# Kernel tuning notes

Hardware: AMD Instinct MI355X
Metric: run time of the kernel (lower is better)

Reference implementation:

```python
import jax, jax.numpy as jnp
import numpy as np

N = 131072   # active input voxels (stride=1 -> same output voxels)
K = 27       # 3x3x3 kernel offsets
P = 32768    # padded kernel-map pairs per offset
CIN = 64
COUT = 64


def setup_inputs() -> dict:
    key = jax.random.key(0)
    kf, kw, kb, ki, ko, km = jax.random.split(key, 6)
    features = jax.random.normal(kf, (N, CIN), jnp.float32)
    weight = jax.random.normal(kw, (K, CIN, COUT), jnp.float32) * 0.05
    bias = jax.random.normal(kb, (COUT,), jnp.float32)
    # kernel map: per-offset (input_row, output_row) pairs, -1 = padding
    in_map = jax.random.randint(ki, (K, P), 0, N, dtype=jnp.int32)
    out_map = jax.random.randint(ko, (K, P), 0, N, dtype=jnp.int32)
    valid = jax.random.uniform(km, (K, P)) < 0.8
    in_map = jnp.where(valid, in_map, -1)
    out_map = jnp.where(valid, out_map, -1)
    return {"features": features, "weight": weight, "bias": bias,
            "in_map": in_map, "out_map": out_map}


def reference(features, weight, bias, in_map, out_map):
    # Sparse conv = per-offset gather -> GEMM -> scatter-add, plus bias.
    valid = in_map >= 0                                   # [K, P]
    safe_in = jnp.where(valid, in_map, 0)
    gathered = features[safe_in] * valid[:, :, None].astype(features.dtype)  # [K,P,Cin]
    y = jnp.einsum('kpi,kio->kpo', gathered, weight)      # [K,P,Cout]
    safe_out = jnp.where(valid, out_map, 0).reshape(-1)   # invalid rows carry zeros
    out = jnp.zeros((features.shape[0], weight.shape[-1]), features.dtype)
    out = out.at[safe_out].add(y.reshape(-1, weight.shape[-1]))
    return out + bias[None, :]
```

## Files before the change

kernel.cpp:

```cpp
#include <hip/hip_runtime.h>
#include <hip/hip_bf16.h>

#define NVOX 131072
#define KOFF 27
#define PPAIR 32768
#define CIN 64
#define COUT 64
#define PPB 128
#define FS 72
#define TOTP (KOFF * PPAIR)
#define CAP 12
#define OVF_MAX 32768

typedef __attribute__((ext_vector_type(8))) short bf16x8;
typedef __attribute__((ext_vector_type(4))) float f32x4;
typedef __attribute__((ext_vector_type(4))) unsigned int u32x4;
typedef __attribute__((ext_vector_type(2))) unsigned int u32x2;

static constexpr size_t WIMG_BYTES = (size_t)KOFF * COUT * FS * 2;
static constexpr size_t FB_BYTES   = ((size_t)NVOX + 1) * CIN * 2;

static constexpr size_t YC_OFF    = 0;
static constexpr size_t YC_BYTES  = (size_t)NVOX * CAP * COUT * 2;
static constexpr size_t CUR2_OFF  = YC_OFF + YC_BYTES;
static constexpr size_t OVFC_OFF  = CUR2_OFF + (size_t)NVOX * 4;
static constexpr size_t OVF_OFF   = OVFC_OFF + 256;
static constexpr size_t WIMG2_OFF = OVF_OFF + (size_t)OVF_MAX * 4;
static constexpr size_t FB2_OFF   = (WIMG2_OFF + WIMG_BYTES + 255) & ~(size_t)255;
static constexpr size_t WS_CAP    = FB2_OFF + FB_BYTES;

static constexpr size_t Y_OFF     = 0;
static constexpr size_t Y_BYTES   = (size_t)TOTP * COUT * 2;
static constexpr size_t RANK_OFF  = Y_OFF + Y_BYTES;
static constexpr size_t CNT_OFF   = RANK_OFF + (size_t)TOTP * 4;
static constexpr size_t START_OFF = CNT_OFF + (size_t)NVOX * 4;
static constexpr size_t BSUM_OFF  = START_OFF + ((size_t)NVOX + 64) * 4;
static constexpr size_t BOFF_OFF  = BSUM_OFF + 512 * 4;
static constexpr size_t WIMG_OFF  = BOFF_OFF + 520 * 4;
static constexpr size_t FB_OFF    = (WIMG_OFF + WIMG_BYTES + 255) & ~(size_t)255;
static constexpr size_t WS_FULL   = FB_OFF + FB_BYTES;

__device__ __forceinline__ unsigned short f2bf(float f) {
    union { __hip_bfloat16 h; unsigned short u; } v;
    v.h = __float2bfloat16(f);
    return v.u;
}
__device__ __forceinline__ float bfbits2f(unsigned int u) {
    union { unsigned int i; float f; } v; v.i = u << 16; return v.f;
}
__device__ __forceinline__ float dot8(u32x4 a, u32x4 b) {
    float s = 0.f;
    s += bfbits2f(a.x & 0xffffu) * bfbits2f(b.x & 0xffffu);
    s += bfbits2f(a.x >> 16)     * bfbits2f(b.x >> 16);
    s += bfbits2f(a.y & 0xffffu) * bfbits2f(b.y & 0xffffu);
    s += bfbits2f(a.y >> 16)     * bfbits2f(b.y >> 16);
    s += bfbits2f(a.z & 0xffffu) * bfbits2f(b.z & 0xffffu);
    s += bfbits2f(a.z >> 16)     * bfbits2f(b.z >> 16);
    s += bfbits2f(a.w & 0xffffu) * bfbits2f(b.w & 0xffffu);
    s += bfbits2f(a.w >> 16)     * bfbits2f(b.w >> 16);
    return s;
}

#define NB_F2B 4096
#define NB_WP  KOFF
#define NB_RNK (TOTP / 256)

__global__ __launch_bounds__(256) void prep2_kernel(
    const float* __restrict__ f, unsigned short* __restrict__ fb,
    const float* __restrict__ w, unsigned short* __restrict__ wimg)
{
    const int bid = blockIdx.x;
    const int tid = threadIdx.x;
    if (bid < NB_F2B) {
        int i = bid * 256 + tid;
        float4 a = ((const float4*)f)[i * 2];
        float4 b = ((const float4*)f)[i * 2 + 1];
        union { u32x4 u; unsigned short s[8]; } pk;
        pk.s[0]=f2bf(a.x); pk.s[1]=f2bf(a.y); pk.s[2]=f2bf(a.z); pk.s[3]=f2bf(a.w);
        pk.s[4]=f2bf(b.x); pk.s[5]=f2bf(b.y); pk.s[6]=f2bf(b.z); pk.s[7]=f2bf(b.w);
        ((u32x4*)fb)[i] = pk.u;
    } else {
        const int k    = bid - NB_F2B;
        const int cout = tid & 63;
        const int ci0  = (tid >> 6) * 16;
        const float* wk = w + (size_t)k * CIN * COUT;
        union { u32x4 u[2]; unsigned short s[16]; } pk;
#pragma unroll
        for (int i = 0; i < 16; ++i)
            pk.s[i] = f2bf(wk[(ci0 + i) * COUT + cout]);
        unsigned short* dst = wimg + (size_t)k * COUT * FS + cout * FS + ci0;
        *(u32x4*)dst       = pk.u[0];
        *(u32x4*)(dst + 8) = pk.u[1];
        if (k == 0 && tid < CIN) fb[(size_t)NVOX * CIN + tid] = 0;
    }
}

__global__ __launch_bounds__(256) void conv5_kernel(
    const unsigned short* __restrict__ featbf,
    const unsigned short* __restrict__ wimg,
    const int* __restrict__ in_map,
    const int* __restrict__ out_map,
    int* __restrict__ cursor,
    int* __restrict__ ovf_cnt,
    int* __restrict__ ovf,
    unsigned short* __restrict__ Ybf)
{
    __shared__ unsigned short Fl[PPB * FS];
    __shared__ unsigned short Wt[COUT * FS];

    const int tid  = threadIdx.x;
    const int wave = tid >> 6;
    const int lane = tid & 63;
    const int k    = blockIdx.x >> 8;
    const int pb   = blockIdx.x & 255;
    const int base = k * PPAIR + pb * PPB;

    const int p = tid >> 1;
    const int h = tid & 1;
    int slot = -1;
    {
        int o = out_map[base + p];
        if (h == 0 && o >= 0) {
            int r0 = atomicAdd(&cursor[o], 1);
            if (r0 < CAP) {
                slot = o * CAP + r0;
            } else {
                int idx = atomicAdd(ovf_cnt, 1);
                if (idx < OVF_MAX) ovf[idx] = base + p;
            }
        }
    }

    {
        const unsigned short* wsrc = wimg + (size_t)k * COUT * FS;
        for (int c = wave; c < 9; c += 4)
            __builtin_amdgcn_global_load_lds(
                (const __attribute__((address_space(1))) void*)(wsrc + c * 512 + lane * 8),
                (__attribute__((address_space(3))) void*)(&Wt[c * 512 + lane * 8]),
                16, 0, 0);
    }

    {
        int im = in_map[base + p];
        const u32x4* src = (const u32x4*)(featbf + (size_t)(im >= 0 ? im : NVOX) * CIN + h * 32);
        u32x4 v0 = src[0], v1 = src[1], v2 = src[2], v3 = src[3];
        u32x4* dst = (u32x4*)&Fl[p * FS + h * 32];
        dst[0] = v0; dst[1] = v1; dst[2] = v2; dst[3] = v3;
    }

    slot = __shfl(slot, lane & 62);

    __syncthreads();

    const int r = lane & 15;
    const int g = lane >> 4;

    bf16x8 af[2][2];
    bf16x8 bfr[4][2];
#pragma unroll
    for (int m = 0; m < 2; ++m)
#pragma unroll
        for (int s = 0; s < 2; ++s)
            af[m][s] = *(const bf16x8*)&Fl[(wave * 32 + m * 16 + r) * FS + s * 32 + g * 8];
#pragma unroll
    for (int n = 0; n < 4; ++n)
#pragma unroll
        for (int s = 0; s < 2; ++s)
            bfr[n][s] = *(const bf16x8*)&Wt[(n * 16 + r) * FS + s * 32 + g * 8];

    f32x4 acc[2][4];
#pragma unroll
    for (int m = 0; m < 2; ++m)
#pragma unroll
        for (int n = 0; n < 4; ++n)
            acc[m][n] = (f32x4){0.f, 0.f, 0.f, 0.f};

#pragma unroll
    for (int s = 0; s < 2; ++s)
#pragma unroll
        for (int m = 0; m < 2; ++m)
#pragma unroll
            for (int n = 0; n < 4; ++n)
                acc[m][n] = __builtin_amdgcn_mfma_f32_16x16x32_bf16(
                    af[m][s], bfr[n][s], acc[m][n], 0, 0, 0);

#pragma unroll
    for (int m = 0; m < 2; ++m)
#pragma unroll
        for (int n = 0; n < 4; ++n)
#pragma unroll
            for (int j = 0; j < 4; ++j)
                Fl[(wave * 32 + m * 16 + g * 4 + j) * FS + n * 16 + r] = f2bf(acc[m][n][j]);

    if (slot >= 0) {
        const unsigned short* src = &Fl[p * FS + h * 32];
        u32x4* dst = (u32x4*)(Ybf + (size_t)slot * COUT + h * 32);
        u32x4 v0 = *(const u32x4*)(src + 0);
        u32x4 v1 = *(const u32x4*)(src + 8);
        u32x4 v2 = *(const u32x4*)(src + 16);
        u32x4 v3 = *(const u32x4*)(src + 24);
        dst[0] = v0; dst[1] = v1; dst[2] = v2; dst[3] = v3;
    }
}

__global__ __launch_bounds__(256) void gather_cap_kernel(
    const unsigned short* __restrict__ Y,
    const int* __restrict__ cursor,
    const float* __restrict__ bias,
    float* __restrict__ out)
{
    const int row  = blockIdx.x * 4 + (threadIdx.x >> 6);
    const int lane = threadIdx.x & 63;
    const int c4   = (lane & 15) * 4;
    const int grp  = lane >> 4;

    int cnt = cursor[row];
    if (cnt > CAP) cnt = CAP;
    const unsigned short* yb = Y + (size_t)row * CAP * COUT;

    float4 acc = {0.f, 0.f, 0.f, 0.f};
    for (int j = grp; j < cnt; j += 4) {
        u32x2 v = *(const u32x2*)&yb[j * COUT + c4];
        acc.x += bfbits2f(v.x & 0xffffu);
        acc.y += bfbits2f(v.x >> 16);
        acc.z += bfbits2f(v.y & 0xffffu);
        acc.w += bfbits2f(v.y >> 16);
    }
    acc.x += __shfl_xor(acc.x, 16); acc.y += __shfl_xor(acc.y, 16);
    acc.z += __shfl_xor(acc.z, 16); acc.w += __shfl_xor(acc.w, 16);
    acc.x += __shfl_xor(acc.x, 32); acc.y += __shfl_xor(acc.y, 32);
    acc.z += __shfl_xor(acc.z, 32); acc.w += __shfl_xor(acc.w, 32);

    if (grp == 0) {
        float4 b = *(const float4*)&bias[c4];
        float4 rv = {acc.x + b.x, acc.y + b.y, acc.z + b.z, acc.w + b.w};
        *(float4*)&out[(size_t)row * COUT + c4] = rv;
    }
}

__global__ __launch_bounds__(256) void fixup_kernel(
    const unsigned short* __restrict__ fb,
    const unsigned short* __restrict__ wimg,
    const int* __restrict__ in_map,
    const int* __restrict__ out_map,
    const int* __restrict__ ovf_cnt,
    const int* __restrict__ ovf,
    float* __restrict__ out)
{
    int n = ovf_cnt[0];
    if (n > OVF_MAX) n = OVF_MAX;
    const int lane = threadIdx.x & 63;
    const int wid  = (blockIdx.x * 256 + threadIdx.x) >> 6;
    const int nw   = (gridDim.x * 256) >> 6;
    for (int e = wid; e < n; e += nw) {
        int t  = ovf[e];
        int k  = t >> 15;
        int in = in_map[t];
        int o  = out_map[t];
        const u32x4* fr = (const u32x4*)(fb + (size_t)in * CIN);
        const unsigned short* wr = wimg + (size_t)k * COUT * FS + lane * FS;
        float acc = 0.f;
#pragma unroll
        for (int c8 = 0; c8 < 8; ++c8)
            acc += dot8(fr[c8], *(const u32x4*)(wr + c8 * 8));
        unsafeAtomicAdd(out + (size_t)o * COUT + lane, acc);
    }
}

__global__ __launch_bounds__(256) void prep_kernel(
    const float* __restrict__ f, unsigned short* __restrict__ fb,
    const float* __restrict__ w, unsigned short* __restrict__ wimg,
    const int* __restrict__ out_map, int* __restrict__ counts,
    int* __restrict__ rank)
{
    const int bid = blockIdx.x;
    const int tid = threadIdx.x;
    if (bid < NB_F2B) {
        int i = bid * 256 + tid;
        float4 a = ((const float4*)f)[i * 2];
        float4 b = ((const float4*)f)[i * 2 + 1];
        union { u32x4 u; unsigned short s[8]; } pk;
        pk.s[0]=f2bf(a.x); pk.s[1]=f2bf(a.y); pk.s[2]=f2bf(a.z); pk.s[3]=f2bf(a.w);
        pk.s[4]=f2bf(b.x); pk.s[5]=f2bf(b.y); pk.s[6]=f2bf(b.z); pk.s[7]=f2bf(b.w);
        ((u32x4*)fb)[i] = pk.u;
    } else if (bid < NB_F2B + NB_WP) {
        const int k    = bid - NB_F2B;
        const int cout = tid & 63;
        const int ci0  = (tid >> 6) * 16;
        const float* wk = w + (size_t)k * CIN * COUT;
        union { u32x4 u[2]; unsigned short s[16]; } pk;
#pragma unroll
        for (int i = 0; i < 16; ++i)
            pk.s[i] = f2bf(wk[(ci0 + i) * COUT + cout]);
        unsigned short* dst = wimg + (size_t)k * COUT * FS + cout * FS + ci0;
        *(u32x4*)dst       = pk.u[0];
        *(u32x4*)(dst + 8) = pk.u[1];
        if (k == 0 && tid < CIN) fb[(size_t)NVOX * CIN + tid] = 0;
    } else {
        int t = (bid - NB_F2B - NB_WP) * 256 + tid;
        int o = out_map[t];
        rank[t] = (o >= 0) ? atomicAdd(&counts[o], 1) : -1;
    }
}

__global__ void scan1_kernel(const int* __restrict__ counts, int* __restrict__ startv,
                             int* __restrict__ bsum) {
    __shared__ int sm[256];
    int gid = blockIdx.x * 256 + threadIdx.x;
    int v = counts[gid];
    sm[threadIdx.x] = v;
    __syncthreads();
    for (int off = 1; off < 256; off <<= 1) {
        int t = (threadIdx.x >= off) ? sm[threadIdx.x - off] : 0;
        __syncthreads();
        sm[threadIdx.x] += t;
        __syncthreads();
    }
    int incl = sm[threadIdx.x];
    startv[gid] = incl - v;
    if (threadIdx.x == 255) bsum[blockIdx.x] = incl;
}

__global__ void scan2_kernel(const int* __restrict__ bsum, int* __restrict__ boff) {
    __shared__ int sm[512];
    int v = bsum[threadIdx.x];
    sm[threadIdx.x] = v;
    __syncthreads();
    for (int off = 1; off < 512; off <<= 1) {
        int t = (threadIdx.x >= off) ? sm[threadIdx.x - off] : 0;
        __syncthreads();
        sm[threadIdx.x] += t;
        __syncthreads();
    }
    boff[threadIdx.x] = sm[threadIdx.x] - v;
    if (threadIdx.x == 511) boff[512] = sm[511];
}

__global__ __launch_bounds__(256) void conv4_kernel(
    const unsigned short* __restrict__ featbf,
    const unsigned short* __restrict__ wimg,
    const int* __restrict__ in_map,
    const int* __restrict__ out_map,
    const int* __restrict__ startv,
    const int* __restrict__ boff,
    const int* __restrict__ rank,
    unsigned short* __restrict__ Ybf)
{
    __shared__ unsigned short Fl[PPB * FS];
    __shared__ unsigned short Wt[COUT * FS];

    const int tid  = threadIdx.x;
    const int wave = tid >> 6;
    const int lane = tid & 63;
    const int k    = blockIdx.x >> 8;
    const int pb   = blockIdx.x & 255;
    const int base = k * PPAIR + pb * PPB;

    {
        const unsigned short* wsrc = wimg + (size_t)k * COUT * FS;
        for (int c = wave; c < 9; c += 4)
            __builtin_amdgcn_global_load_lds(
                (const __attribute__((address_space(1))) void*)(wsrc + c * 512 + lane * 8),
                (__attribute__((address_space(3))) void*)(&Wt[c * 512 + lane * 8]),
                16, 0, 0);
    }
    {
        const int row = tid >> 1;
        const int h   = tid & 1;
        int im = in_map[base + row];
        const u32x4* src = (const u32x4*)(featbf + (size_t)(im >= 0 ? im : NVOX) * CIN + h * 32);
        u32x4 v0 = src[0], v1 = src[1], v2 = src[2], v3 = src[3];
        u32x4* dst = (u32x4*)&Fl[row * FS + h * 32];
        dst[0] = v0; dst[1] = v1; dst[2] = v2; dst[3] = v3;
    }
    __syncthreads();

    const int r = lane & 15;
    const int g = lane >> 4;

    bf16x8 af[2][2];
    bf16x8 bfr[4][2];
#pragma unroll
    for (int m = 0; m < 2; ++m)
#pragma unroll
        for (int s = 0; s < 2; ++s)
            af[m][s] = *(const bf16x8*)&Fl[(wave * 32 + m * 16 + r) * FS + s * 32 + g * 8];
#pragma unroll
    for (int n = 0; n < 4; ++n)
#pragma unroll
        for (int s = 0; s < 2; ++s)
            bfr[n][s] = *(const bf16x8*)&Wt[(n * 16 + r) * FS + s * 32 + g * 8];

    f32x4 acc[2][4];
#pragma unroll
    for (int m = 0; m < 2; ++m)
#pragma unroll
        for (int n = 0; n < 4; ++n)
            acc[m][n] = (f32x4){0.f, 0.f, 0.f, 0.f};

#pragma unroll
    for (int s = 0; s < 2; ++s)
#pragma unroll
        for (int m = 0; m < 2; ++m)
#pragma unroll
            for (int n = 0; n < 4; ++n)
                acc[m][n] = __builtin_amdgcn_mfma_f32_16x16x32_bf16(
                    af[m][s], bfr[n][s], acc[m][n], 0, 0, 0);

#pragma unroll
    for (int m = 0; m < 2; ++m)
#pragma unroll
        for (int n = 0; n < 4; ++n)
#pragma unroll
            for (int j = 0; j < 4; ++j)
                Fl[(wave * 32 + m * 16 + g * 4 + j) * FS + n * 16 + r] = f2bf(acc[m][n][j]);

    {
        const int p = tid >> 1;
        const int h = tid & 1;
        int o = out_map[base + p];
        if (o >= 0) {
            int s = startv[o] + boff[o >> 8] + rank[base + p];
            const unsigned short* src = &Fl[p * FS + h * 32];
            u32x4* dst = (u32x4*)(Ybf + (size_t)s * COUT + h * 32);
            u32x4 v0 = *(const u32x4*)(src + 0);
            u32x4 v1 = *(const u32x4*)(src + 8);
            u32x4 v2 = *(const u32x4*)(src + 16);
            u32x4 v3 = *(const u32x4*)(src + 24);
            dst[0] = v0; dst[1] = v1; dst[2] = v2; dst[3] = v3;
        }
    }
}

__global__ __launch_bounds__(256) void gather_out_kernel(
    const unsigned short* __restrict__ Y,
    const int* __restrict__ startv,
    const int* __restrict__ boff,
    const float* __restrict__ bias,
    float* __restrict__ out)
{
    const int row  = blockIdx.x * 4 + (threadIdx.x >> 6);
    const int lane = threadIdx.x & 63;
    const int c4   = (lane & 15) * 4;
    const int grp  = lane >> 4;

    const int b0 = row >> 8;
    int s0 = startv[row] + boff[b0];
    int s1 = ((row + 1) & 255) ? (startv[row + 1] + boff[b0]) : boff[b0 + 1];

    float4 acc = {0.f, 0.f, 0.f, 0.f};
    for (int j = s0 + grp; j < s1; j += 4) {
        u32x2 v = *(const u32x2*)&Y[(size_t)j * COUT + c4];
        acc.x += bfbits2f(v.x & 0xffffu);
        acc.y += bfbits2f(v.x >> 16);
        acc.z += bfbits2f(v.y & 0xffffu);
        acc.w += bfbits2f(v.y >> 16);
    }
    acc.x += __shfl_xor(acc.x, 16); acc.y += __shfl_xor(acc.y, 16);
    acc.z += __shfl_xor(acc.z, 16); acc.w += __shfl_xor(acc.w, 16);
    acc.x += __shfl_xor(acc.x, 32); acc.y += __shfl_xor(acc.y, 32);
    acc.z += __shfl_xor(acc.z, 32); acc.w += __shfl_xor(acc.w, 32);

    if (grp == 0) {
        float4 b = *(const float4*)&bias[c4];
        float4 rv = {acc.x + b.x, acc.y + b.y, acc.z + b.z, acc.w + b.w};
        *(float4*)&out[(size_t)row * COUT + c4] = rv;
    }
}

__global__ void init_out_kernel(float* __restrict__ out, const float* __restrict__ bias) {
    int i = blockIdx.x * blockDim.x + threadIdx.x;
    float4 b = ((const float4*)bias)[i & 15];
    ((float4*)out)[i] = b;
}

__global__ __launch_bounds__(256) void conv_atomic_kernel(
    const float* __restrict__ features, const float* __restrict__ weight,
    const int* __restrict__ in_map, const int* __restrict__ out_map,
    float* __restrict__ out)
{
    __shared__ float Wl[CIN * COUT];
    __shared__ float Fl2[128 * 65];
    const int tid = threadIdx.x;
    const int k = blockIdx.x / (PPAIR / 128);
    const int pb = blockIdx.x % (PPAIR / 128);
    const int base = k * PPAIR + pb * 128;
    const float* wk = weight + k * CIN * COUT;
#pragma unroll
    for (int j = 0; j < 4; ++j) {
        int idx = (j * 256 + tid) * 4;
        *(float4*)&Wl[idx] = *(const float4*)&wk[idx];
    }
    const int lane = tid & 63;
    const int rsel = tid >> 6;
#pragma unroll 4
    for (int j = 0; j < 128; j += 4) {
        int row = j + rsel;
        int in_row = in_map[base + row];
        float v = 0.0f;
        if (in_row >= 0) v = features[in_row * CIN + lane];
        Fl2[row * 65 + lane] = v;
    }
    __syncthreads();
    const int cg = tid & 7;
    const int pg = tid >> 3;
    float acc[4][8];
#pragma unroll
    for (int a = 0; a < 4; ++a)
#pragma unroll
        for (int b = 0; b < 8; ++b) acc[a][b] = 0.0f;
    const float* wbase = &Wl[cg * 8];
    const float* fbase = &Fl2[pg * 4 * 65];
#pragma unroll 8
    for (int i = 0; i < CIN; ++i) {
        float4 w0 = *(const float4*)&wbase[i * 64];
        float4 w1 = *(const float4*)&wbase[i * 64 + 4];
        float wv[8] = {w0.x, w0.y, w0.z, w0.w, w1.x, w1.y, w1.z, w1.w};
        float fv[4];
#pragma unroll
        for (int a = 0; a < 4; ++a) fv[a] = fbase[a * 65 + i];
#pragma unroll
        for (int a = 0; a < 4; ++a)
#pragma unroll
            for (int b = 0; b < 8; ++b)
                acc[a][b] = fmaf(fv[a], wv[b], acc[a][b]);
    }
#pragma unroll
    for (int a = 0; a < 4; ++a) {
        int pair = pg * 4 + a;
        int orow = out_map[base + pair];
        if (orow >= 0) {
            float* dst = out + orow * COUT + cg * 8;
#pragma unroll
            for (int b = 0; b < 8; ++b) unsafeAtomicAdd(dst + b, acc[a][b]);
        }
    }
}

extern "C" void kernel_launch(void* const* d_in, const int* in_sizes, int n_in,
                              void* d_out, int out_size, void* d_ws, size_t ws_size,
                              hipStream_t stream) {
    const float* features = (const float*)d_in[0];
    const float* weight   = (const float*)d_in[1];
    const float* bias     = (const float*)d_in[2];
    const int*   in_map   = (const int*)d_in[3];
    const int*   out_map  = (const int*)d_in[4];
    float*       out      = (float*)d_out;
    char* ws = (char*)d_ws;

    if (ws_size >= WS_CAP) {
        unsigned short* Ybf  = (unsigned short*)(ws + YC_OFF);
        int* cursor  = (int*)(ws + CUR2_OFF);
        int* ovf_cnt = (int*)(ws + OVFC_OFF);
        int* ovf     = (int*)(ws + OVF_OFF);
        unsigned short* wimg = (unsigned short*)(ws + WIMG2_OFF);
        unsigned short* fb   = (unsigned short*)(ws + FB2_OFF);

        (void)hipMemsetAsync(cursor, 0, (size_t)NVOX * 4, stream);
        (void)hipMemsetAsync(ovf_cnt, 0, 256, stream);

        prep2_kernel<<<NB_F2B + NB_WP, 256, 0, stream>>>(features, fb, weight, wimg);
        conv5_kernel<<<KOFF * 256, 256, 0, stream>>>(
            fb, wimg, in_map, out_map, cursor, ovf_cnt, ovf, Ybf);
        gather_cap_kernel<<<NVOX / 4, 256, 0, stream>>>(Ybf, cursor, bias, out);
        fixup_kernel<<<256, 256, 0, stream>>>(fb, wimg, in_map, out_map, ovf_cnt, ovf, out);
        return;
    }

    if (ws_size >= WS_FULL) {
        unsigned short* Ybf  = (unsigned short*)(ws + Y_OFF);
        int* rank   = (int*)(ws + RANK_OFF);
        int* counts = (int*)(ws + CNT_OFF);
        int* startv = (int*)(ws + START_OFF);
        int* bsum   = (int*)(ws + BSUM_OFF);
        int* boff   = (int*)(ws + BOFF_OFF);
        unsigned short* wimg = (unsigned short*)(ws + WIMG_OFF);
        unsigned short* fb   = (unsigned short*)(ws + FB_OFF);

        (void)hipMemsetAsync(counts, 0, (size_t)NVOX * 4, stream);
        prep_kernel<<<NB_F2B + NB_WP + NB_RNK, 256, 0, stream>>>(
            features, fb, weight, wimg, out_map, counts, rank);
        scan1_kernel<<<NVOX / 256, 256, 0, stream>>>(counts, startv, bsum);
        scan2_kernel<<<1, 512, 0, stream>>>(bsum, boff);
        conv4_kernel<<<KOFF * 256, 256, 0, stream>>>(
            fb, wimg, in_map, out_map, startv, boff, rank, Ybf);
        gather_out_kernel<<<NVOX / 4, 256, 0, stream>>>(Ybf, startv, boff, bias, out);
        return;
    }

    int total4 = NVOX * COUT / 4;
    init_out_kernel<<<total4 / 256, 256, 0, stream>>>(out, bias);
    conv_atomic_kernel<<<KOFF * (PPAIR / 128), 256, 0, stream>>>(
        features, weight, in_map, out_map, out);
}
```

Before: 112.7 us.

## Pre-swizzle weights into MFMA fragment layout and read them straight from global

```diff
diff --git a/kernel.cpp b/kernel.cpp
--- a/kernel.cpp
+++ b/kernel.cpp
@@ -67,12 +67,15 @@
 
 __global__ __launch_bounds__(256) void prep2_kernel(
     const float* __restrict__ f, unsigned short* __restrict__ fb,
-    const float* __restrict__ w, unsigned short* __restrict__ wimg)
+    const float* __restrict__ w, unsigned short* __restrict__ wimg2,
+    int* __restrict__ cursor, int* __restrict__ ovf_cnt)
 {
     const int bid = blockIdx.x;
     const int tid = threadIdx.x;
     if (bid < NB_F2B) {
         int i = bid * 256 + tid;
+        if (bid < 128) ((u32x4*)cursor)[i] = (u32x4){0, 0, 0, 0};
+        if (bid == 128 && tid == 0) ovf_cnt[0] = 0;
         float4 a = ((const float4*)f)[i * 2];
         float4 b = ((const float4*)f)[i * 2 + 1];
         union { u32x4 u; unsigned short s[8]; } pk;
@@ -80,24 +83,29 @@
         pk.s[4]=f2bf(b.x); pk.s[5]=f2bf(b.y); pk.s[6]=f2bf(b.z); pk.s[7]=f2bf(b.w);
         ((u32x4*)fb)[i] = pk.u;
     } else {
-        const int k    = bid - NB_F2B;
-        const int cout = tid & 63;
-        const int ci0  = (tid >> 6) * 16;
+        const int k = bid - NB_F2B;
+        const int n = tid >> 6;
+        const int l = tid & 63;
+        const int r = l & 15;
+        const int g = l >> 4;
+        const int cout = n * 16 + r;
         const float* wk = w + (size_t)k * CIN * COUT;
-        union { u32x4 u[2]; unsigned short s[16]; } pk;
-#pragma unroll
-        for (int i = 0; i < 16; ++i)
-            pk.s[i] = f2bf(wk[(ci0 + i) * COUT + cout]);
-        unsigned short* dst = wimg + (size_t)k * COUT * FS + cout * FS + ci0;
-        *(u32x4*)dst       = pk.u[0];
-        *(u32x4*)(dst + 8) = pk.u[1];
+#pragma unroll
+        for (int s = 0; s < 2; ++s) {
+            const int ci0 = s * 32 + g * 8;
+            union { u32x4 u; unsigned short sh[8]; } pk;
+#pragma unroll
+            for (int j = 0; j < 8; ++j)
+                pk.sh[j] = f2bf(wk[(ci0 + j) * COUT + cout]);
+            *(u32x4*)(wimg2 + (size_t)k * 4096 + ((n * 2 + s) * 64 + l) * 8) = pk.u;
+        }
         if (k == 0 && tid < CIN) fb[(size_t)NVOX * CIN + tid] = 0;
     }
 }
 
-__global__ __launch_bounds__(256) void conv5_kernel(
+__global__ __launch_bounds__(256, 6) void conv6_kernel(
     const unsigned short* __restrict__ featbf,
-    const unsigned short* __restrict__ wimg,
+    const unsigned short* __restrict__ wimg2,
     const int* __restrict__ in_map,
     const int* __restrict__ out_map,
     int* __restrict__ cursor,
@@ -106,7 +114,6 @@
     unsigned short* __restrict__ Ybf)
 {
     __shared__ unsigned short Fl[PPB * FS];
-    __shared__ unsigned short Wt[COUT * FS];
 
     const int tid  = threadIdx.x;
     const int wave = tid >> 6;
@@ -117,56 +124,41 @@
 
     const int p = tid >> 1;
     const int h = tid & 1;
+
+    int im = in_map[base + p];
+    int o  = out_map[base + p];
+    const u32x4* src = (const u32x4*)(featbf + (size_t)(im >= 0 ? im : NVOX) * CIN + h * 32);
+    u32x4 v0 = src[0], v1 = src[1], v2 = src[2], v3 = src[3];
+
     int slot = -1;
+    if (h == 0 && o >= 0) {
+        int r0 = atomicAdd(&cursor[o], 1);
+        if (r0 < CAP) {
+            slot = o * CAP + r0;
+        } else {
+            int idx = atomicAdd(ovf_cnt, 1);
+            if (idx < OVF_MAX) ovf[idx] = base + p;
+        }
+    }
+    slot = __shfl(slot, lane & 62);
+
     {
-        int o = out_map[base + p];
-        if (h == 0 && o >= 0) {
-            int r0 = atomicAdd(&cursor[o], 1);
-            if (r0 < CAP) {
-                slot = o * CAP + r0;
-            } else {
-                int idx = atomicAdd(ovf_cnt, 1);
-                if (idx < OVF_MAX) ovf[idx] = base + p;
-            }
-        }
-    }
-
-    {
-        const unsigned short* wsrc = wimg + (size_t)k * COUT * FS;
-        for (int c = wave; c < 9; c += 4)
-            __builtin_amdgcn_global_load_lds(
-                (const __attribute__((address_space(1))) void*)(wsrc + c * 512 + lane * 8),
-                (__attribute__((address_space(3))) void*)(&Wt[c * 512 + lane * 8]),
-                16, 0, 0);
-    }
-
-    {
-        int im = in_map[base + p];
-        const u32x4* src = (const u32x4*)(featbf + (size_t)(im >= 0 ? im : NVOX) * CIN + h * 32);
-        u32x4 v0 = src[0], v1 = src[1], v2 = src[2], v3 = src[3];
         u32x4* dst = (u32x4*)&Fl[p * FS + h * 32];
         dst[0] = v0; dst[1] = v1; dst[2] = v2; dst[3] = v3;
     }
-
-    slot = __shfl(slot, lane & 62);
-
     __syncthreads();
 
     const int r = lane & 15;
     const int g = lane >> 4;
 
     bf16x8 af[2][2];
-    bf16x8 bfr[4][2];
 #pragma unroll
     for (int m = 0; m < 2; ++m)
 #pragma unroll
         for (int s = 0; s < 2; ++s)
             af[m][s] = *(const bf16x8*)&Fl[(wave * 32 + m * 16 + r) * FS + s * 32 + g * 8];
-#pragma unroll
-    for (int n = 0; n < 4; ++n)
-#pragma unroll
-        for (int s = 0; s < 2; ++s)
-            bfr[n][s] = *(const bf16x8*)&Wt[(n * 16 + r) * FS + s * 32 + g * 8];
+
+    const unsigned short* wk2 = wimg2 + (size_t)k * 4096 + (size_t)lane * 8;
 
     f32x4 acc[2][4];
 #pragma unroll
@@ -178,11 +170,13 @@
 #pragma unroll
     for (int s = 0; s < 2; ++s)
 #pragma unroll
-        for (int m = 0; m < 2; ++m)
-#pragma unroll
-            for (int n = 0; n < 4; ++n)
+        for (int n = 0; n < 4; ++n) {
+            bf16x8 b = *(const bf16x8*)(wk2 + (size_t)(n * 2 + s) * 512);
+#pragma unroll
+            for (int m = 0; m < 2; ++m)
                 acc[m][n] = __builtin_amdgcn_mfma_f32_16x16x32_bf16(
-                    af[m][s], bfr[n][s], acc[m][n], 0, 0, 0);
+                    af[m][s], b, acc[m][n], 0, 0, 0);
+        }
 
 #pragma unroll
     for (int m = 0; m < 2; ++m)
@@ -193,13 +187,13 @@
                 Fl[(wave * 32 + m * 16 + g * 4 + j) * FS + n * 16 + r] = f2bf(acc[m][n][j]);
 
     if (slot >= 0) {
-        const unsigned short* src = &Fl[p * FS + h * 32];
+        const unsigned short* csrc = &Fl[p * FS + h * 32];
         u32x4* dst = (u32x4*)(Ybf + (size_t)slot * COUT + h * 32);
-        u32x4 v0 = *(const u32x4*)(src + 0);
-        u32x4 v1 = *(const u32x4*)(src + 8);
-        u32x4 v2 = *(const u32x4*)(src + 16);
-        u32x4 v3 = *(const u32x4*)(src + 24);
-        dst[0] = v0; dst[1] = v1; dst[2] = v2; dst[3] = v3;
+        u32x4 w0 = *(const u32x4*)(csrc + 0);
+        u32x4 w1 = *(const u32x4*)(csrc + 8);
+        u32x4 w2 = *(const u32x4*)(csrc + 16);
+        u32x4 w3 = *(const u32x4*)(csrc + 24);
+        dst[0] = w0; dst[1] = w1; dst[2] = w2; dst[3] = w3;
     }
 }
 
@@ -240,7 +234,7 @@
 
 __global__ __launch_bounds__(256) void fixup_kernel(
     const unsigned short* __restrict__ fb,
-    const unsigned short* __restrict__ wimg,
+    const unsigned short* __restrict__ wimg2,
     const int* __restrict__ in_map,
     const int* __restrict__ out_map,
     const int* __restrict__ ovf_cnt,
@@ -252,17 +246,23 @@
     const int lane = threadIdx.x & 63;
     const int wid  = (blockIdx.x * 256 + threadIdx.x) >> 6;
     const int nw   = (gridDim.x * 256) >> 6;
+    const int nn   = lane >> 4;
+    const int rr   = lane & 15;
     for (int e = wid; e < n; e += nw) {
         int t  = ovf[e];
         int k  = t >> 15;
         int in = in_map[t];
         int o  = out_map[t];
         const u32x4* fr = (const u32x4*)(fb + (size_t)in * CIN);
-        const unsigned short* wr = wimg + (size_t)k * COUT * FS + lane * FS;
+        const unsigned short* wk2 = wimg2 + (size_t)k * 4096;
         float acc = 0.f;
 #pragma unroll
-        for (int c8 = 0; c8 < 8; ++c8)
-            acc += dot8(fr[c8], *(const u32x4*)(wr + c8 * 8));
+        for (int s = 0; s < 2; ++s)
+#pragma unroll
+            for (int g = 0; g < 4; ++g) {
+                u32x4 wc = *(const u32x4*)(wk2 + ((nn * 2 + s) * 64 + g * 16 + rr) * 8);
+                acc += dot8(fr[s * 4 + g], wc);
+            }
         unsafeAtomicAdd(out + (size_t)o * COUT + lane, acc);
     }
 }
@@ -549,21 +549,19 @@
     char* ws = (char*)d_ws;
 
     if (ws_size >= WS_CAP) {
-        unsigned short* Ybf  = (unsigned short*)(ws + YC_OFF);
+        unsigned short* Ybf   = (unsigned short*)(ws + YC_OFF);
         int* cursor  = (int*)(ws + CUR2_OFF);
         int* ovf_cnt = (int*)(ws + OVFC_OFF);
         int* ovf     = (int*)(ws + OVF_OFF);
-        unsigned short* wimg = (unsigned short*)(ws + WIMG2_OFF);
-        unsigned short* fb   = (unsigned short*)(ws + FB2_OFF);
-
-        (void)hipMemsetAsync(cursor, 0, (size_t)NVOX * 4, stream);
-        (void)hipMemsetAsync(ovf_cnt, 0, 256, stream);
-
-        prep2_kernel<<<NB_F2B + NB_WP, 256, 0, stream>>>(features, fb, weight, wimg);
-        conv5_kernel<<<KOFF * 256, 256, 0, stream>>>(
-            fb, wimg, in_map, out_map, cursor, ovf_cnt, ovf, Ybf);
+        unsigned short* wimg2 = (unsigned short*)(ws + WIMG2_OFF);
+        unsigned short* fb    = (unsigned short*)(ws + FB2_OFF);
+
+        prep2_kernel<<<NB_F2B + NB_WP, 256, 0, stream>>>(
+            features, fb, weight, wimg2, cursor, ovf_cnt);
+        conv6_kernel<<<KOFF * 256, 256, 0, stream>>>(
+            fb, wimg2, in_map, out_map, cursor, ovf_cnt, ovf, Ybf);
         gather_cap_kernel<<<NVOX / 4, 256, 0, stream>>>(Ybf, cursor, bias, out);
-        fixup_kernel<<<256, 256, 0, stream>>>(fb, wimg, in_map, out_map, ovf_cnt, ovf, out);
+        fixup_kernel<<<256, 256, 0, stream>>>(fb, wimg2, in_map, out_map, ovf_cnt, ovf, out);
         return;
     }
 
```

New measurement: 99.71 us. -11.5%, faster.
